# Performance work log

Hardware: AMD Instinct MI355X
Metric: run time of the kernel (lower is better)

## Reference

```python
import math
import jax, jax.numpy as jnp
import numpy as np

H = 8      # num_heads
K = 3      # polynomial order
WH, WW = 8, 8  # win_size


def _relative_position_index(wh, ww):
    coords = np.stack(np.meshgrid(np.arange(wh), np.arange(ww), indexing='ij'))  # [2,wh,ww]
    cf = coords.reshape(2, -1)                       # [2, N]
    rel = cf[:, :, None] - cf[:, None, :]            # [2, N, N]
    rel = rel.transpose(1, 2, 0).astype(np.int64)    # [N, N, 2]
    rel[..., 0] += wh - 1
    rel[..., 1] += ww - 1
    rel[..., 0] *= 2 * ww - 1
    return rel.sum(-1)                               # [N, N]


def setup_inputs() -> dict:
    key = jax.random.key(0)
    ks = jax.random.split(key, 10)
    B, N, C = 1024, WH * WW, 256
    hd = C // H
    s = 0.02
    inp = {
        'x': jax.random.normal(ks[0], (B, N, C), dtype=jnp.float32),
        'Wq': jax.random.normal(ks[1], (C, C), dtype=jnp.float32) * s,
        'bq': jnp.zeros((C,), dtype=jnp.float32),
        'Wkv': jax.random.normal(ks[2], (C, 2 * C), dtype=jnp.float32) * s,
        'bkv': jnp.zeros((2 * C,), dtype=jnp.float32),
        'Wgate': jax.random.normal(ks[3], (hd, K + 1), dtype=jnp.float32) * s,
        'bgate': jnp.zeros((K + 1,), dtype=jnp.float32),
        'Wproj': jax.random.normal(ks[4], (C, C), dtype=jnp.float32) * s,
        'bproj': jnp.zeros((C,), dtype=jnp.float32),
        'bias_table': jax.random.normal(ks[5], ((2 * WH - 1) * (2 * WW - 1), H), dtype=jnp.float32) * s,
        'rel_index': jnp.asarray(_relative_position_index(WH, WW)),
    }
    return inp


def reference(x, Wq, bq, Wkv, bkv, Wgate, bgate, Wproj, bproj, bias_table, rel_index):
    B, N, C = x.shape
    hd = C // H
    # per-(batch,head) sigmoid gates over the K+1 polynomial orders
    gate = jax.nn.sigmoid(x.mean(axis=1).reshape(B, H, hd) @ Wgate + bgate)  # [B,H,K+1]
    gate = gate[..., None, None]                                             # [B,H,K+1,1,1]

    q = (x @ Wq + bq).reshape(B, N, H, hd).transpose(0, 2, 1, 3)             # [B,H,N,hd]
    kv = (x @ Wkv + bkv).reshape(B, N, 2, H, hd).transpose(2, 0, 3, 1, 4)
    k, v = kv[0], kv[1]                                                      # [B,H,N,hd]

    q = jax.nn.softmax(q, axis=-1)
    k = jax.nn.softmax(k, axis=-1)
    attn = jnp.einsum('bhnd,bhmd->bhnm', q, k)                               # [B,H,N,N] (>=0)

    bias = bias_table[rel_index.reshape(-1)].reshape(N, N, H).transpose(2, 0, 1)  # [H,N,N]
    attn = attn + jax.nn.relu(bias)[None]
    attn = (attn + attn.transpose(0, 1, 3, 2)) * 0.5

    # symmetric degree normalization: D^{-1/2} A D^{-1/2}, zero-degree rows untouched
    d = attn.sum(axis=-1)                                                    # [B,H,N]
    dn = jnp.where(d > 0, 1.0 / jnp.sqrt(jnp.where(d > 0, d, 1.0)), d)
    attn = attn * dn[:, :, None, :] * dn[:, :, :, None]

    I = jnp.eye(N, dtype=attn.dtype)
    L = I - attn        # Laplacian
    L_hat = I + attn    # 2I - L

    # tmp[i] = L_hat^i (tmp[0] = I broadcasts)
    tmp = [I]
    E = I
    for _ in range(K):
        E = E @ L_hat
        tmp.append(E)

    c = [math.comb(K, j) / 2 ** K for j in range(K + 1)]
    out = c[0] * gate[:, :, K] * (tmp[K] @ v)                                # [B,H,N,hd]
    E = I
    for j in range(K):
        E = E @ L
        out = out + c[j + 1] * gate[:, :, j] * (E @ (tmp[K - j - 1] @ v))

    out = out.transpose(0, 2, 1, 3).reshape(B, N, C)
    out = out @ Wproj + bproj
    return out
```

## Files before the change

### kernel.cpp

```cpp
#include <hip/hip_runtime.h>
#include <hip/hip_bf16.h>

typedef __attribute__((ext_vector_type(8))) short bf16x8;
typedef __attribute__((ext_vector_type(4))) float f32x4;

__device__ __forceinline__ unsigned short f2bf(float f) {
    union { __hip_bfloat16 h; unsigned short u; } c;
    c.h = __float2bfloat16(f);
    return c.u;
}
__device__ __forceinline__ unsigned int pk2(float lo, float hi) {
    return (unsigned int)f2bf(lo) | ((unsigned int)f2bf(hi) << 16);
}
__device__ __forceinline__ bf16x8 as_bf(uint4 u) {
    union { uint4 a; bf16x8 b; } c; c.a = u; return c.b;
}
__device__ __forceinline__ float bf2f(unsigned short us) {
    return __uint_as_float(((unsigned int)us) << 16);
}
__device__ __forceinline__ void gload_lds16(const void* g, void* l) {
    __builtin_amdgcn_global_load_lds(
        (const __attribute__((address_space(1))) void*)g,
        (__attribute__((address_space(3))) void*)l, 16, 0, 0);
}

__global__ __launch_bounds__(256) void prep_kernel(
    const float* __restrict__ x,
    const float* __restrict__ Wq, const float* __restrict__ Wkv, const float* __restrict__ Wproj,
    const float* __restrict__ Wgate, const float* __restrict__ bgate,
    const float* __restrict__ bias_table, const int* __restrict__ rel_index,
    unsigned short* __restrict__ xbf, int use_xbf,
    unsigned short* __restrict__ wq, unsigned short* __restrict__ wk,
    unsigned short* __restrict__ wv, unsigned short* __restrict__ wp,
    float* __restrict__ bsym, float* __restrict__ wpoly)
{
    const int bid = blockIdx.x, t = threadIdx.x;
    if (bid < 1024) {
        __shared__ float ps[8][256];
        __shared__ float mean_s[256];
        __shared__ float gsig[32];
        const int b = (bid & 7) * 128 + (bid >> 3);
        const float* xb = x + (size_t)b * 16384;
        if (use_xbf) {
            unsigned short* xo = xbf + (size_t)b * 16384;
            const int cg = t & 31, rr = t >> 5;
            float cs[8] = {};
            #pragma unroll
            for (int i = 0; i < 8; i++) {
                int row = rr * 8 + i;
                const float4* p = (const float4*)(xb + row * 256 + cg * 8);
                float4 f0 = p[0], f1 = p[1];
                uint4 u;
                u.x = pk2(f0.x, f0.y); u.y = pk2(f0.z, f0.w);
                u.z = pk2(f1.x, f1.y); u.w = pk2(f1.z, f1.w);
                *(uint4*)(xo + row * 256 + cg * 8) = u;
                cs[0] += f0.x; cs[1] += f0.y; cs[2] += f0.z; cs[3] += f0.w;
                cs[4] += f1.x; cs[5] += f1.y; cs[6] += f1.z; cs[7] += f1.w;
            }
            #pragma unroll
            for (int j = 0; j < 8; j++) ps[rr][cg * 8 + j] = cs[j];
            __syncthreads();
            float s = 0.f;
            #pragma unroll
            for (int r8 = 0; r8 < 8; r8++) s += ps[r8][t];
            mean_s[t] = s * (1.f / 64.f);
        } else {
            float s = 0.f;
            #pragma unroll 8
            for (int n = 0; n < 64; n++) s += xb[n * 256 + t];
            mean_s[t] = s * (1.f / 64.f);
        }
        __syncthreads();
        if (t < 32) {
            int h = t >> 2, j = t & 3;
            float g = bgate[j];
            #pragma unroll 8
            for (int dd = 0; dd < 32; dd++) g = fmaf(mean_s[h * 32 + dd], Wgate[dd * 4 + j], g);
            gsig[t] = 1.f / (1.f + __expf(-g));
        }
        __syncthreads();
        if (t < 8) {
            float g0 = gsig[t * 4], g1 = gsig[t * 4 + 1], g2 = gsig[t * 4 + 2], g3 = gsig[t * 4 + 3];
            float a = 0.125f * g3, bb = 0.375f * g0, cc = 0.375f * g1, dd = 0.125f * g2;
            float4 o;
            o.x = a + bb + cc + dd;
            o.y = 3.f * a + bb - cc - 3.f * dd;
            o.z = 3.f * a - bb - cc + 3.f * dd;
            o.w = a - bb + cc - dd;
            ((float4*)wpoly)[b * 8 + t] = o;
        }
    } else if (bid < 2048) {
        int e = (bid - 1024) * 256 + t;
        int m = e >> 16, r = e & 65535, o = r >> 8, kk = r & 255;
        float v; unsigned short* dst;
        if (m == 0)      { v = Wq[kk * 256 + o];        dst = wq; }
        else if (m == 1) { v = Wkv[kk * 512 + o];       dst = wk; }
        else if (m == 2) { v = Wkv[kk * 512 + 256 + o]; dst = wv; }
        else             { v = Wproj[kk * 256 + o];     dst = wp; }
        dst[o * 256 + kk] = f2bf(v);
    } else {
        int e = (bid - 2048) * 256 + t;
        int hh = e >> 12, ij = e & 4095;
        int i = ij >> 6, j = ij & 63;
        float bij = bias_table[rel_index[ij] * 8 + hh];
        float bji = bias_table[rel_index[j * 64 + i] * 8 + hh];
        bsym[hh * 4096 + ij] = 0.5f * (fmaxf(bij, 0.f) + fmaxf(bji, 0.f));
    }
}

template <bool XBF>
__global__ __launch_bounds__(256, 4) void attn_kernel(
    const float* __restrict__ x, const unsigned short* __restrict__ xbf,
    const float* __restrict__ bq, const float* __restrict__ bkv,
    const unsigned short* __restrict__ wq, const unsigned short* __restrict__ wk,
    const unsigned short* __restrict__ wv,
    const float* __restrict__ bsym, const float* __restrict__ wpoly,
    unsigned short* __restrict__ hid)
{
    __shared__ __align__(16) unsigned char tile[32768];
    float* dn = (float*)(tile + 28672);

    const int bid = blockIdx.x;
    const int xcd = bid & 7, idx = bid >> 3;
    const int b = xcd * 128 + (idx >> 3), h = idx & 7;
    const int t = threadIdx.x;
    const int l = t & 63, w = t >> 6;
    const int lr = l & 15, qg = l >> 4;

    const float4 wv4 = ((const float4*)wpoly)[b * 8 + h];

    const int role = w;
    uint4 Bfr0[8], Bfr1[8];
    {
        const unsigned short* wsel = (role == 0) ? wq : (role == 1) ? wk : wv;
        const uint4* Wp = (const uint4*)wsel;
        const int ct0 = (role < 2) ? 0 : (role - 2);
        const int o0 = h * 32 + ct0 * 16 + lr;
        #pragma unroll
        for (int ks = 0; ks < 8; ks++) Bfr0[ks] = Wp[o0 * 32 + ks * 4 + qg];
        if (role < 2) {
            #pragma unroll
            for (int ks = 0; ks < 8; ks++) Bfr1[ks] = Wp[(o0 + 16) * 32 + ks * 4 + qg];
        }
    }

    if (XBF) {
        const unsigned short* xb = xbf + (size_t)b * 16384;
        const int rp = l >> 5, u = l & 31;
        #pragma unroll
        for (int i = 0; i < 8; i++) {
            int row = i * 8 + w * 2 + rp;
            int csrc = (u & 24) | ((u & 7) ^ (row & 7));
            gload_lds16(xb + row * 256 + csrc * 8, tile + (i * 8 + w * 2) * 512);
        }
    } else {
        const float* xb = x + (size_t)b * 16384;
        #pragma unroll
        for (int i = 0; i < 8; i++) {
            int e = t + i * 256;
            int row = e >> 5, c = e & 31;
            const float4* p = (const float4*)(xb + row * 256 + c * 8);
            float4 f0 = p[0], f1 = p[1];
            uint4 u;
            u.x = pk2(f0.x, f0.y); u.y = pk2(f0.z, f0.w);
            u.z = pk2(f1.x, f1.y); u.w = pk2(f1.z, f1.w);
            *(uint4*)(tile + row * 512 + ((c >> 3) << 7) + (((c & 7) ^ (row & 7)) << 4)) = u;
        }
    }

    f32x4 acc0[4], acc1[4];
    {
        const int ct0 = (role < 2) ? 0 : (role - 2);
        const int o0 = h * 32 + ct0 * 16 + lr;
        float b0 = (role == 0) ? bq[o0] : (role == 1) ? bkv[o0] : bkv[256 + o0];
        float b1 = (role == 0) ? bq[o0 + 16] : (role == 1) ? bkv[o0 + 16] : 0.f;
        #pragma unroll
        for (int mt = 0; mt < 4; mt++) {
            f32x4 z0 = {b0, b0, b0, b0}; acc0[mt] = z0;
            f32x4 z1 = {b1, b1, b1, b1}; acc1[mt] = z1;
        }
    }
    __syncthreads();

    __builtin_amdgcn_s_setprio(1);
    if (role < 2) {
        #pragma unroll
        for (int mt = 0; mt < 4; mt++) {
            const int rowA = mt * 16 + lr;
            #pragma unroll
            for (int ks = 0; ks < 8; ks++) {
                const int c = ks * 4 + qg;
                bf16x8 af = *(const bf16x8*)(tile + rowA * 512 + ((c >> 3) << 7) + (((c & 7) ^ (rowA & 7)) << 4));
                acc0[mt] = __builtin_amdgcn_mfma_f32_16x16x32_bf16(af, as_bf(Bfr0[ks]), acc0[mt], 0, 0, 0);
                acc1[mt] = __builtin_amdgcn_mfma_f32_16x16x32_bf16(af, as_bf(Bfr1[ks]), acc1[mt], 0, 0, 0);
            }
        }
    } else {
        #pragma unroll
        for (int mt = 0; mt < 4; mt++) {
            const int rowA = mt * 16 + lr;
            #pragma unroll
            for (int ks = 0; ks < 8; ks++) {
                const int c = ks * 4 + qg;
                bf16x8 af = *(const bf16x8*)(tile + rowA * 512 + ((c >> 3) << 7) + (((c & 7) ^ (rowA & 7)) << 4));
                acc0[mt] = __builtin_amdgcn_mfma_f32_16x16x32_bf16(af, as_bf(Bfr0[ks]), acc0[mt], 0, 0, 0);
            }
        }
    }
    __builtin_amdgcn_s_setprio(0);
    __syncthreads();

    float bsv[4][4];
    {
        const float* bh_ = bsym + h * 4096;
        #pragma unroll
        for (int jt = 0; jt < 4; jt++)
            #pragma unroll
            for (int r = 0; r < 4; r++)
                bsv[jt][r] = bh_[(w * 16 + qg * 4 + r) * 64 + jt * 16 + lr];
    }

    if (role < 2) {
        #pragma unroll
        for (int mt = 0; mt < 4; mt++)
            #pragma unroll
            for (int r = 0; r < 4; r++) {
                float e0 = __expf(acc0[mt][r]), e1 = __expf(acc1[mt][r]);
                float s = e0 + e1;
                s += __shfl_xor(s, 1); s += __shfl_xor(s, 2);
                s += __shfl_xor(s, 4); s += __shfl_xor(s, 8);
                float inv = 1.f / s;
                acc0[mt][r] = e0 * inv; acc1[mt][r] = e1 * inv;
            }
    }

    if (role == 0) {
        #pragma unroll
        for (int mt = 0; mt < 4; mt++)
            #pragma unroll
            for (int r = 0; r < 4; r++) {
                int row = mt * 16 + qg * 4 + r;
                int d0 = lr, d1 = 16 + lr;
                *(short*)(tile + row * 128 + (((d0 >> 3) ^ (row & 7)) << 4) + (d0 & 7) * 2) = (short)f2bf(acc0[mt][r]);
                *(short*)(tile + row * 128 + (((d1 >> 3) ^ (row & 7)) << 4) + (d1 & 7) * 2) = (short)f2bf(acc1[mt][r]);
            }
    } else if (role == 1) {
        #pragma unroll
        for (int mt = 0; mt < 4; mt++)
            #pragma unroll
            for (int r = 0; r < 4; r++) {
                int row = mt * 16 + qg * 4 + r;
                int d0 = lr, d1 = 16 + lr;
                *(short*)(tile + 8192 + row * 128 + (((d0 >> 3) ^ (row & 7)) << 4) + (d0 & 7) * 2) = (short)f2bf(acc0[mt][r]);
                *(short*)(tile + 8192 + row * 128 + (((d1 >> 3) ^ (row & 7)) << 4) + (d1 & 7) * 2) = (short)f2bf(acc1[mt][r]);
            }
    } else {
        const int d = (role - 2) * 16 + lr;
        #pragma unroll
        for (int mt = 0; mt < 4; mt++)
            #pragma unroll
            for (int r = 0; r < 4; r++) {
                int row = mt * 16 + qg * 4 + r;
                *(short*)(tile + 16384 + d * 128 + (((row >> 3) ^ (d & 7)) << 4) + (row & 7) * 2) = (short)f2bf(acc0[mt][r]);
            }
    }
    __syncthreads();

    float sv[4][4];
    float dnv[4];
    {
        const int swz = (qg ^ (lr & 7)) << 4;
        bf16x8 aqf = *(const bf16x8*)(tile + (w * 16 + lr) * 128 + swz);
        bf16x8 akf = *(const bf16x8*)(tile + 8192 + (w * 16 + lr) * 128 + swz);
        float rs[4] = {0.f, 0.f, 0.f, 0.f};
        __builtin_amdgcn_s_setprio(1);
        #pragma unroll
        for (int jt = 0; jt < 4; jt++) {
            bf16x8 bqf = *(const bf16x8*)(tile + (jt * 16 + lr) * 128 + swz);
            bf16x8 bkf = *(const bf16x8*)(tile + 8192 + (jt * 16 + lr) * 128 + swz);
            f32x4 qk = {0.f, 0.f, 0.f, 0.f}, kq = {0.f, 0.f, 0.f, 0.f};
            qk = __builtin_amdgcn_mfma_f32_16x16x32_bf16(aqf, bkf, qk, 0, 0, 0);
            kq = __builtin_amdgcn_mfma_f32_16x16x32_bf16(akf, bqf, kq, 0, 0, 0);
            #pragma unroll
            for (int r = 0; r < 4; r++) {
                float v = 0.5f * (qk[r] + kq[r]) + bsv[jt][r];
                sv[jt][r] = v;
                rs[r] += v;
            }
        }
        __builtin_amdgcn_s_setprio(0);
        #pragma unroll
        for (int r = 0; r < 4; r++) {
            float s = rs[r];
            s += __shfl_xor(s, 1); s += __shfl_xor(s, 2);
            s += __shfl_xor(s, 4); s += __shfl_xor(s, 8);
            dnv[r] = (s > 0.f) ? rsqrtf(s) : s;
        }
        if (lr == 0) {
            int base = w * 16 + qg * 4;
            dn[base + 0] = dnv[0]; dn[base + 1] = dnv[1];
            dn[base + 2] = dnv[2]; dn[base + 3] = dnv[3];
        }
    }
    __syncthreads();

    {
        float dnj[4];
        #pragma unroll
        for (int jt = 0; jt < 4; jt++) dnj[jt] = dn[jt * 16 + lr];
        #pragma unroll
        for (int jt = 0; jt < 4; jt++)
            #pragma unroll
            for (int r = 0; r < 4; r++) {
                int i = w * 16 + qg * 4 + r, j = jt * 16 + lr;
                *(short*)(tile + i * 128 + (((j >> 3) ^ (i & 7)) << 4) + (j & 7) * 2)
                    = (short)f2bf(sv[jt][r] * dnv[r] * dnj[jt]);
            }
    }
    __syncthreads();

    const float w0c = wv4.x, w1c = wv4.y, w2c = wv4.z, w3c = wv4.w;
    f32x4 y[2];
    #pragma unroll
    for (int ct = 0; ct < 2; ct++)
        #pragma unroll
        for (int r = 0; r < 4; r++) {
            int row = w * 16 + qg * 4 + r;
            int d = ct * 16 + lr;
            unsigned short us = *(unsigned short*)(tile + 16384 + d * 128 + (((row >> 3) ^ (d & 7)) << 4) + (row & 7) * 2);
            y[ct][r] = w0c * bf2f(us);
        }

#define AU_ROUND(SRC, DST, WC, WRITE) {                                                          \
    f32x4 u0 = {0.f,0.f,0.f,0.f}, u1 = {0.f,0.f,0.f,0.f};                                        \
    __builtin_amdgcn_s_setprio(1);                                                               \
    _Pragma("unroll")                                                                            \
    for (int ks2 = 0; ks2 < 2; ks2++) {                                                          \
        int c = ks2 * 4 + qg;                                                                    \
        bf16x8 af = *(const bf16x8*)(tile + (w * 16 + lr) * 128 + ((c ^ (lr & 7)) << 4));        \
        bf16x8 b0 = *(const bf16x8*)(tile + (SRC) + lr * 128 + ((c ^ (lr & 7)) << 4));           \
        bf16x8 b1 = *(const bf16x8*)(tile + (SRC) + (16 + lr) * 128 + ((c ^ (lr & 7)) << 4));    \
        u0 = __builtin_amdgcn_mfma_f32_16x16x32_bf16(af, b0, u0, 0, 0, 0);                       \
        u1 = __builtin_amdgcn_mfma_f32_16x16x32_bf16(af, b1, u1, 0, 0, 0);                       \
    }                                                                                            \
    __builtin_amdgcn_s_setprio(0);                                                               \
    y[0] += (WC) * u0; y[1] += (WC) * u1;                                                        \
    if (WRITE) {                                                                                 \
        _Pragma("unroll")                                                                        \
        for (int r = 0; r < 4; r++) {                                                            \
            int i = w * 16 + qg * 4 + r;                                                         \
            *(short*)(tile + (DST) + lr * 128 + (((i >> 3) ^ (lr & 7)) << 4) + (i & 7) * 2) = (short)f2bf(u0[r]); \
            *(short*)(tile + (DST) + (16 + lr) * 128 + (((i >> 3) ^ (lr & 7)) << 4) + (i & 7) * 2) = (short)f2bf(u1[r]); \
        }                                                                                        \
    }                                                                                            \
    __syncthreads();                                                                             \
}
    AU_ROUND(16384, 20480, w1c, 1)
    AU_ROUND(20480, 24576, w2c, 1)
    AU_ROUND(24576, 0,     w3c, 0)
#undef AU_ROUND

    #pragma unroll
    for (int ct = 0; ct < 2; ct++)
        #pragma unroll
        for (int r = 0; r < 4; r++) {
            int row = w * 16 + qg * 4 + r;
            int col = h * 32 + ct * 16 + lr;
            hid[((size_t)b * 64 + row) * 256 + col] = f2bf(y[ct][r]);
        }
}

__global__ __launch_bounds__(256) void proj_kernel(
    const unsigned short* __restrict__ hidden,
    const unsigned short* __restrict__ wp,
    const float* __restrict__ bproj,
    float* __restrict__ out)
{
    const int bid = blockIdx.x;
    const int rb = (bid & 7) * 64 + (bid >> 3);
    const int t = threadIdx.x, l = t & 63, w = t >> 6;
    const int lr = l & 15, qg = l >> 4;

    const unsigned short* hb = hidden + (size_t)rb * 128 * 256;

    bf16x8 af[2][8];
    #pragma unroll
    for (int rt = 0; rt < 2; rt++) {
        int row = w * 32 + rt * 16 + lr;
        #pragma unroll
        for (int ks = 0; ks < 8; ks++)
            af[rt][ks] = *(const bf16x8*)(hb + row * 256 + (ks * 4 + qg) * 8);
    }
    float bzv[16];
    #pragma unroll
    for (int ct = 0; ct < 16; ct++) bzv[ct] = bproj[ct * 16 + lr];

    const uint4* WP = (const uint4*)wp;
    #pragma unroll 2
    for (int ct = 0; ct < 16; ct++) {
        f32x4 a0 = {0.f, 0.f, 0.f, 0.f}, a1 = {0.f, 0.f, 0.f, 0.f};
        #pragma unroll
        for (int ks = 0; ks < 8; ks++) {
            bf16x8 bf = as_bf(WP[(ct * 16 + lr) * 32 + ks * 4 + qg]);
            a0 = __builtin_amdgcn_mfma_f32_16x16x32_bf16(af[0][ks], bf, a0, 0, 0, 0);
            a1 = __builtin_amdgcn_mfma_f32_16x16x32_bf16(af[1][ks], bf, a1, 0, 0, 0);
        }
        int colg = ct * 16 + lr;
        float bz = bzv[ct];
        #pragma unroll
        for (int r = 0; r < 4; r++) {
            int rowg = rb * 128 + w * 32 + qg * 4 + r;
            out[(size_t)rowg * 256 + colg] = a0[r] + bz;
            out[(size_t)(rowg + 16) * 256 + colg] = a1[r] + bz;
        }
    }
}

extern "C" void kernel_launch(void* const* d_in, const int* in_sizes, int n_in,
                              void* d_out, int out_size, void* d_ws, size_t ws_size,
                              hipStream_t stream) {
    const float* x          = (const float*)d_in[0];
    const float* Wq         = (const float*)d_in[1];
    const float* bq         = (const float*)d_in[2];
    const float* Wkv        = (const float*)d_in[3];
    const float* bkv        = (const float*)d_in[4];
    const float* Wgate      = (const float*)d_in[5];
    const float* bgate      = (const float*)d_in[6];
    const float* Wproj      = (const float*)d_in[7];
    const float* bproj      = (const float*)d_in[8];
    const float* bias_table = (const float*)d_in[9];
    const int*   rel_index  = (const int*)d_in[10];
    float* out = (float*)d_out;
    unsigned char* wsb = (unsigned char*)d_ws;

    const size_t HID   = 0;
    const size_t WQo   = 33554432;
    const size_t WKo   = WQo + 131072;
    const size_t WVo   = WKo + 131072;
    const size_t WPo   = WVo + 131072;
    const size_t BIASo = WPo + 131072;
    const size_t WPOLY = BIASo + 131072;
    const size_t XBFo  = WPOLY + 131072;
    const int use_xbf  = (ws_size >= XBFo + 33554432ull) ? 1 : 0;

    unsigned short* hid = (unsigned short*)(wsb + HID);
    unsigned short* wq  = (unsigned short*)(wsb + WQo);
    unsigned short* wk  = (unsigned short*)(wsb + WKo);
    unsigned short* wv  = (unsigned short*)(wsb + WVo);
    unsigned short* wp  = (unsigned short*)(wsb + WPo);
    float* bsym  = (float*)(wsb + BIASo);
    float* wpoly = (float*)(wsb + WPOLY);
    unsigned short* xbf = (unsigned short*)(wsb + XBFo);

    prep_kernel<<<dim3(2176), dim3(256), 0, stream>>>(
        x, Wq, Wkv, Wproj, Wgate, bgate, bias_table, rel_index,
        xbf, use_xbf, wq, wk, wv, wp, bsym, wpoly);
    if (use_xbf)
        attn_kernel<true><<<dim3(8192), dim3(256), 0, stream>>>(
            x, xbf, bq, bkv, wq, wk, wv, bsym, wpoly, hid);
    else
        attn_kernel<false><<<dim3(8192), dim3(256), 0, stream>>>(
            x, xbf, bq, bkv, wq, wk, wv, bsym, wpoly, hid);
    proj_kernel<<<dim3(512), dim3(256), 0, stream>>>(hid, wp, bproj, out);
}
```

Before: 145.9 us.

## Process two heads per 512-thread block sharing one staged x tile

Each attention block now handles two heads of the same batch element with 512 threads instead of one head with 256. The bf16 x tile is loaded into LDS once and reused for both heads' Q/K/V projections, halving x staging traffic and block count. Per-head LDS regions are laid out separately, with an extra XOR swizzle on the shared Q/K area, and LDS per block grows to about 41KB. The cost is larger blocks with more LDS and launch bounds of 512x4, which may lower occupancy or raise register pressure.

```diff
diff --git a/kernel.cpp b/kernel.cpp
--- a/kernel.cpp
+++ b/kernel.cpp
@@ -109,7 +109,7 @@
 }
 
 template <bool XBF>
-__global__ __launch_bounds__(256, 4) void attn_kernel(
+__global__ __launch_bounds__(512, 4) void attn_kernel(
     const float* __restrict__ x, const unsigned short* __restrict__ xbf,
     const float* __restrict__ bq, const float* __restrict__ bkv,
     const unsigned short* __restrict__ wq, const unsigned short* __restrict__ wk,
@@ -117,28 +117,37 @@
     const float* __restrict__ bsym, const float* __restrict__ wpoly,
     unsigned short* __restrict__ hid)
 {
-    __shared__ __align__(16) unsigned char tile[32768];
-    float* dn = (float*)(tile + 28672);
+    __shared__ __align__(16) unsigned char tile[41472];
 
     const int bid = blockIdx.x;
     const int xcd = bid & 7, idx = bid >> 3;
-    const int b = xcd * 128 + (idx >> 3), h = idx & 7;
+    const int b = xcd * 128 + (idx >> 2);
+    const int hp = idx & 3;
     const int t = threadIdx.x;
     const int l = t & 63, w = t >> 6;
     const int lr = l & 15, qg = l >> 4;
+    const int hl = w >> 2;
+    const int ws = w & 3;
+    const int h  = hp * 2 + hl;
+    const int hs = hl << 2;
+
+    const int AB = hl * 8192;
+    const int VT = 16384 + hl * 4096;
+    const int UA = 24576 + hl * 8192;
+    const int UB = 28672 + hl * 8192;
+    float* dnp = (float*)(tile + 40960 + hl * 256);
 
     const float4 wv4 = ((const float4*)wpoly)[b * 8 + h];
 
-    const int role = w;
     uint4 Bfr0[8], Bfr1[8];
     {
-        const unsigned short* wsel = (role == 0) ? wq : (role == 1) ? wk : wv;
+        const unsigned short* wsel = (ws == 0) ? wq : (ws == 1) ? wk : wv;
         const uint4* Wp = (const uint4*)wsel;
-        const int ct0 = (role < 2) ? 0 : (role - 2);
+        const int ct0 = (ws < 2) ? 0 : (ws - 2);
         const int o0 = h * 32 + ct0 * 16 + lr;
         #pragma unroll
         for (int ks = 0; ks < 8; ks++) Bfr0[ks] = Wp[o0 * 32 + ks * 4 + qg];
-        if (role < 2) {
+        if (ws < 2) {
             #pragma unroll
             for (int ks = 0; ks < 8; ks++) Bfr1[ks] = Wp[(o0 + 16) * 32 + ks * 4 + qg];
         }
@@ -148,16 +157,16 @@
         const unsigned short* xb = xbf + (size_t)b * 16384;
         const int rp = l >> 5, u = l & 31;
         #pragma unroll
-        for (int i = 0; i < 8; i++) {
-            int row = i * 8 + w * 2 + rp;
+        for (int i = 0; i < 4; i++) {
+            int row = i * 16 + w * 2 + rp;
             int csrc = (u & 24) | ((u & 7) ^ (row & 7));
-            gload_lds16(xb + row * 256 + csrc * 8, tile + (i * 8 + w * 2) * 512);
+            gload_lds16(xb + row * 256 + csrc * 8, tile + (i * 16 + w * 2) * 512);
         }
     } else {
         const float* xb = x + (size_t)b * 16384;
         #pragma unroll
-        for (int i = 0; i < 8; i++) {
-            int e = t + i * 256;
+        for (int i = 0; i < 4; i++) {
+            int e = t + i * 512;
             int row = e >> 5, c = e & 31;
             const float4* p = (const float4*)(xb + row * 256 + c * 8);
             float4 f0 = p[0], f1 = p[1];
@@ -170,10 +179,10 @@
 
     f32x4 acc0[4], acc1[4];
     {
-        const int ct0 = (role < 2) ? 0 : (role - 2);
+        const int ct0 = (ws < 2) ? 0 : (ws - 2);
         const int o0 = h * 32 + ct0 * 16 + lr;
-        float b0 = (role == 0) ? bq[o0] : (role == 1) ? bkv[o0] : bkv[256 + o0];
-        float b1 = (role == 0) ? bq[o0 + 16] : (role == 1) ? bkv[o0 + 16] : 0.f;
+        float b0 = (ws == 0) ? bq[o0] : (ws == 1) ? bkv[o0] : bkv[256 + o0];
+        float b1 = (ws == 0) ? bq[o0 + 16] : (ws == 1) ? bkv[o0 + 16] : 0.f;
         #pragma unroll
         for (int mt = 0; mt < 4; mt++) {
             f32x4 z0 = {b0, b0, b0, b0}; acc0[mt] = z0;
@@ -183,7 +192,7 @@
     __syncthreads();
 
     __builtin_amdgcn_s_setprio(1);
-    if (role < 2) {
+    if (ws < 2) {
         #pragma unroll
         for (int mt = 0; mt < 4; mt++) {
             const int rowA = mt * 16 + lr;
@@ -217,10 +226,10 @@
         for (int jt = 0; jt < 4; jt++)
             #pragma unroll
             for (int r = 0; r < 4; r++)
-                bsv[jt][r] = bh_[(w * 16 + qg * 4 + r) * 64 + jt * 16 + lr];
-    }
-
-    if (role < 2) {
+                bsv[jt][r] = bh_[(ws * 16 + qg * 4 + r) * 64 + jt * 16 + lr];
+    }
+
+    if (ws < 2) {
         #pragma unroll
         for (int mt = 0; mt < 4; mt++)
             #pragma unroll
@@ -234,34 +243,34 @@
             }
     }
 
-    if (role == 0) {
+    if (ws == 0) {
         #pragma unroll
         for (int mt = 0; mt < 4; mt++)
             #pragma unroll
             for (int r = 0; r < 4; r++) {
                 int row = mt * 16 + qg * 4 + r;
                 int d0 = lr, d1 = 16 + lr;
-                *(short*)(tile + row * 128 + (((d0 >> 3) ^ (row & 7)) << 4) + (d0 & 7) * 2) = (short)f2bf(acc0[mt][r]);
-                *(short*)(tile + row * 128 + (((d1 >> 3) ^ (row & 7)) << 4) + (d1 & 7) * 2) = (short)f2bf(acc1[mt][r]);
-            }
-    } else if (role == 1) {
+                *(short*)(tile + row * 128 + ((((d0 >> 3) ^ (row & 7)) ^ hs) << 4) + (d0 & 7) * 2) = (short)f2bf(acc0[mt][r]);
+                *(short*)(tile + row * 128 + ((((d1 >> 3) ^ (row & 7)) ^ hs) << 4) + (d1 & 7) * 2) = (short)f2bf(acc1[mt][r]);
+            }
+    } else if (ws == 1) {
         #pragma unroll
         for (int mt = 0; mt < 4; mt++)
             #pragma unroll
             for (int r = 0; r < 4; r++) {
                 int row = mt * 16 + qg * 4 + r;
                 int d0 = lr, d1 = 16 + lr;
-                *(short*)(tile + 8192 + row * 128 + (((d0 >> 3) ^ (row & 7)) << 4) + (d0 & 7) * 2) = (short)f2bf(acc0[mt][r]);
-                *(short*)(tile + 8192 + row * 128 + (((d1 >> 3) ^ (row & 7)) << 4) + (d1 & 7) * 2) = (short)f2bf(acc1[mt][r]);
+                *(short*)(tile + 8192 + row * 128 + ((((d0 >> 3) ^ (row & 7)) ^ hs) << 4) + (d0 & 7) * 2) = (short)f2bf(acc0[mt][r]);
+                *(short*)(tile + 8192 + row * 128 + ((((d1 >> 3) ^ (row & 7)) ^ hs) << 4) + (d1 & 7) * 2) = (short)f2bf(acc1[mt][r]);
             }
     } else {
-        const int d = (role - 2) * 16 + lr;
+        const int d = (ws - 2) * 16 + lr;
         #pragma unroll
         for (int mt = 0; mt < 4; mt++)
             #pragma unroll
             for (int r = 0; r < 4; r++) {
                 int row = mt * 16 + qg * 4 + r;
-                *(short*)(tile + 16384 + d * 128 + (((row >> 3) ^ (d & 7)) << 4) + (row & 7) * 2) = (short)f2bf(acc0[mt][r]);
+                *(short*)(tile + VT + d * 128 + (((row >> 3) ^ (d & 7)) << 4) + (row & 7) * 2) = (short)f2bf(acc0[mt][r]);
             }
     }
     __syncthreads();
@@ -269,9 +278,9 @@
     float sv[4][4];
     float dnv[4];
     {
-        const int swz = (qg ^ (lr & 7)) << 4;
-        bf16x8 aqf = *(const bf16x8*)(tile + (w * 16 + lr) * 128 + swz);
-        bf16x8 akf = *(const bf16x8*)(tile + 8192 + (w * 16 + lr) * 128 + swz);
+        const int swz = ((qg ^ (lr & 7)) ^ hs) << 4;
+        bf16x8 aqf = *(const bf16x8*)(tile + (ws * 16 + lr) * 128 + swz);
+        bf16x8 akf = *(const bf16x8*)(tile + 8192 + (ws * 16 + lr) * 128 + swz);
         float rs[4] = {0.f, 0.f, 0.f, 0.f};
         __builtin_amdgcn_s_setprio(1);
         #pragma unroll
@@ -297,9 +306,9 @@
             dnv[r] = (s > 0.f) ? rsqrtf(s) : s;
         }
         if (lr == 0) {
-            int base = w * 16 + qg * 4;
-            dn[base + 0] = dnv[0]; dn[base + 1] = dnv[1];
-            dn[base + 2] = dnv[2]; dn[base + 3] = dnv[3];
+            int base = ws * 16 + qg * 4;
+            dnp[base + 0] = dnv[0]; dnp[base + 1] = dnv[1];
+            dnp[base + 2] = dnv[2]; dnp[base + 3] = dnv[3];
         }
     }
     __syncthreads();
@@ -307,13 +316,13 @@
     {
         float dnj[4];
         #pragma unroll
-        for (int jt = 0; jt < 4; jt++) dnj[jt] = dn[jt * 16 + lr];
+        for (int jt = 0; jt < 4; jt++) dnj[jt] = dnp[jt * 16 + lr];
         #pragma unroll
         for (int jt = 0; jt < 4; jt++)
             #pragma unroll
             for (int r = 0; r < 4; r++) {
-                int i = w * 16 + qg * 4 + r, j = jt * 16 + lr;
-                *(short*)(tile + i * 128 + (((j >> 3) ^ (i & 7)) << 4) + (j & 7) * 2)
+                int i = ws * 16 + qg * 4 + r, j = jt * 16 + lr;
+                *(short*)(tile + AB + i * 128 + (((j >> 3) ^ (i & 7)) << 4) + (j & 7) * 2)
                     = (short)f2bf(sv[jt][r] * dnv[r] * dnj[jt]);
             }
     }
@@ -325,9 +334,9 @@
     for (int ct = 0; ct < 2; ct++)
         #pragma unroll
         for (int r = 0; r < 4; r++) {
-            int row = w * 16 + qg * 4 + r;
+            int row = ws * 16 + qg * 4 + r;
             int d = ct * 16 + lr;
-            unsigned short us = *(unsigned short*)(tile + 16384 + d * 128 + (((row >> 3) ^ (d & 7)) << 4) + (row & 7) * 2);
+            unsigned short us = *(unsigned short*)(tile + VT + d * 128 + (((row >> 3) ^ (d & 7)) << 4) + (row & 7) * 2);
             y[ct][r] = w0c * bf2f(us);
         }
 
@@ -337,7 +346,7 @@
     _Pragma("unroll")                                                                            \
     for (int ks2 = 0; ks2 < 2; ks2++) {                                                          \
         int c = ks2 * 4 + qg;                                                                    \
-        bf16x8 af = *(const bf16x8*)(tile + (w * 16 + lr) * 128 + ((c ^ (lr & 7)) << 4));        \
+        bf16x8 af = *(const bf16x8*)(tile + AB + (ws * 16 + lr) * 128 + ((c ^ (lr & 7)) << 4));  \
         bf16x8 b0 = *(const bf16x8*)(tile + (SRC) + lr * 128 + ((c ^ (lr & 7)) << 4));           \
         bf16x8 b1 = *(const bf16x8*)(tile + (SRC) + (16 + lr) * 128 + ((c ^ (lr & 7)) << 4));    \
         u0 = __builtin_amdgcn_mfma_f32_16x16x32_bf16(af, b0, u0, 0, 0, 0);                       \
@@ -348,23 +357,23 @@
     if (WRITE) {                                                                                 \
         _Pragma("unroll")                                                                        \
         for (int r = 0; r < 4; r++) {                                                            \
-            int i = w * 16 + qg * 4 + r;                                                         \
+            int i = ws * 16 + qg * 4 + r;                                                        \
             *(short*)(tile + (DST) + lr * 128 + (((i >> 3) ^ (lr & 7)) << 4) + (i & 7) * 2) = (short)f2bf(u0[r]); \
             *(short*)(tile + (DST) + (16 + lr) * 128 + (((i >> 3) ^ (lr & 7)) << 4) + (i & 7) * 2) = (short)f2bf(u1[r]); \
         }                                                                                        \
     }                                                                                            \
     __syncthreads();                                                                             \
 }
-    AU_ROUND(16384, 20480, w1c, 1)
-    AU_ROUND(20480, 24576, w2c, 1)
-    AU_ROUND(24576, 0,     w3c, 0)
+    AU_ROUND(VT, UA, w1c, 1)
+    AU_ROUND(UA, UB, w2c, 1)
+    AU_ROUND(UB, 0,  w3c, 0)
 #undef AU_ROUND
 
     #pragma unroll
     for (int ct = 0; ct < 2; ct++)
         #pragma unroll
         for (int r = 0; r < 4; r++) {
-            int row = w * 16 + qg * 4 + r;
+            int row = ws * 16 + qg * 4 + r;
             int col = h * 32 + ct * 16 + lr;
             hid[((size_t)b * 64 + row) * 256 + col] = f2bf(y[ct][r]);
         }
@@ -456,10 +465,10 @@
         x, Wq, Wkv, Wproj, Wgate, bgate, bias_table, rel_index,
         xbf, use_xbf, wq, wk, wv, wp, bsym, wpoly);
     if (use_xbf)
-        attn_kernel<true><<<dim3(8192), dim3(256), 0, stream>>>(
+        attn_kernel<true><<<dim3(4096), dim3(512), 0, stream>>>(
             x, xbf, bq, bkv, wq, wk, wv, bsym, wpoly, hid);
     else
-        attn_kernel<false><<<dim3(8192), dim3(256), 0, stream>>>(
+        attn_kernel<false><<<dim3(4096), dim3(512), 0, stream>>>(
             x, xbf, bq, bkv, wq, wk, wv, bsym, wpoly, hid);
     proj_kernel<<<dim3(512), dim3(256), 0, stream>>>(hid, wp, bproj, out);
 }
```

Result: slower. 159.9 us (+9.6%).
